# Performance work log

Measured on AMD Instinct MI355X. Metric: run time of the kernel, lower is better.

The kernel has to match this reference:

```python
import jax, jax.numpy as jnp
import numpy as np

TOP_K = 2
LN_EPS = 1e-5

B, S, H, E, F = 2, 2048, 1024, 8, 4096


def setup_inputs() -> dict:
    key = jax.random.key(0)
    ks = jax.random.split(key, 6)
    x = jax.random.normal(ks[0], (B, S, H), dtype=jnp.float32)
    Wg = jax.random.normal(ks[1], (H, E), dtype=jnp.float32) * 0.02
    alpha = jax.random.normal(ks[2], (E,), dtype=jnp.float32)
    ln_w = jnp.ones((E, H), dtype=jnp.float32)
    ln_b = jnp.zeros((E, H), dtype=jnp.float32)
    fc1_w = jax.random.normal(ks[3], (E, H, F), dtype=jnp.float32) * 0.02
    fc1_b = jnp.zeros((E, F), dtype=jnp.float32)
    fc2_w = jax.random.normal(ks[4], (E, F, H), dtype=jnp.float32) * 0.02
    fc2_b = jnp.zeros((E, H), dtype=jnp.float32)
    return {"x": x, "Wg": Wg, "alpha": alpha, "ln_w": ln_w, "ln_b": ln_b,
            "fc1_w": fc1_w, "fc1_b": fc1_b, "fc2_w": fc2_w, "fc2_b": fc2_b}


def _layernorm(x, w, b):
    mu = jnp.mean(x, axis=-1, keepdims=True)
    var = jnp.mean(jnp.square(x - mu), axis=-1, keepdims=True)
    return (x - mu) * jax.lax.rsqrt(var + LN_EPS) * w + b


def reference(x, Wg, alpha, ln_w, ln_b, fc1_w, fc1_b, fc2_w, fc2_b):
    b, s, h = x.shape
    xf = x.reshape(-1, h)                                  # [T, H]
    # ---- gate: top-k over expert logits, softmax over the selected k ----
    logits = xf @ Wg                                       # [T, E]
    top_vals, top_idx = jax.lax.top_k(logits, TOP_K)       # [T, K]
    gate_score = jax.nn.softmax(top_vals, axis=-1)         # [T, K]
    # combine weight per (token, expert): sum_k score_k * 1[idx_k == e], scaled by alpha_e
    one_hot = jax.nn.one_hot(top_idx, Wg.shape[1], dtype=xf.dtype)  # [T, K, E]
    comb = jnp.einsum("tke,tk->te", one_hot, gate_score) * alpha    # [T, E]
    # ---- experts: LayerNorm -> fc1 -> gelu(tanh) -> fc2, weighted combine ----
    out = jnp.zeros_like(xf)
    for e in range(Wg.shape[1]):
        hdn = _layernorm(xf, ln_w[e], ln_b[e])
        a = jax.nn.gelu(hdn @ fc1_w[e] + fc1_b[e], approximate=True)
        y = a @ fc2_w[e] + fc2_b[e]
        out = out + y * comb[:, e:e + 1]
    return out.reshape(b, s, h)
```

## Files before the change

kernel.cpp:

```cpp
#include <hip/hip_runtime.h>
#include <stdint.h>
#include <stdio.h>

#define Td 4096
#define Hd 1024
#define Ed 8
#define Fd 4096
#define ROWS_CAP 9216

typedef unsigned int u32;
typedef unsigned short u16;
typedef float f32x4 __attribute__((ext_vector_type(4)));
typedef float f32x2 __attribute__((ext_vector_type(2)));
typedef __bf16 bf16x8 __attribute__((ext_vector_type(8)));
typedef u16 u16x8 __attribute__((ext_vector_type(8)));
typedef u16 u16x4 __attribute__((ext_vector_type(4)));
typedef u32 u32x4 __attribute__((ext_vector_type(4)));

#define ASG __attribute__((address_space(1)))
#define ASL __attribute__((address_space(3)))

__device__ __forceinline__ void gll16(const void* g, void* l) {
  __builtin_amdgcn_global_load_lds((const ASG u32*)g, (ASL u32*)l, 16, 0, 0);
}

__device__ __forceinline__ u16 f2bf(float f) {
  u32 u = __float_as_uint(f);
  u = u + 0x7fffu + ((u >> 16) & 1u);
  return (u16)(u >> 16);
}

__global__ __launch_bounds__(256) void k_gate(const float* __restrict__ x,
    const float* __restrict__ Wg, const float* __restrict__ alpha,
    float* __restrict__ mu, float* __restrict__ rstd,
    int* __restrict__ tok_e, float* __restrict__ tok_w)
{
  const int t = blockIdx.x, tid = threadIdx.x;
  const f32x4 xv = *(const f32x4*)(x + (size_t)t*Hd + tid*4);
  float s1 = 0.f, s2 = 0.f;
  double lg[8];
#pragma unroll
  for (int e=0;e<8;e++) lg[e]=0.0;
#pragma unroll
  for (int i=0;i<4;i++){
    const float xi = xv[i];
    s1 += xi; s2 += xi*xi;
    const f32x4 wa = *(const f32x4*)(Wg + (size_t)(tid*4+i)*Ed);
    const f32x4 wb = *(const f32x4*)(Wg + (size_t)(tid*4+i)*Ed + 4);
    lg[0] += (double)xi*(double)wa[0]; lg[1] += (double)xi*(double)wa[1];
    lg[2] += (double)xi*(double)wa[2]; lg[3] += (double)xi*(double)wa[3];
    lg[4] += (double)xi*(double)wb[0]; lg[5] += (double)xi*(double)wb[1];
    lg[6] += (double)xi*(double)wb[2]; lg[7] += (double)xi*(double)wb[3];
  }
#pragma unroll
  for (int off=32; off>0; off>>=1){
    s1 += __shfl_down(s1, off);
    s2 += __shfl_down(s2, off);
#pragma unroll
    for (int e=0;e<8;e++) lg[e] += __shfl_down(lg[e], off);
  }
  __shared__ double sl[4][8];
  __shared__ float sa[4], sb[4];
  const int w = tid>>6, lane = tid&63;
  if (lane==0){
#pragma unroll
    for (int e=0;e<8;e++) sl[w][e]=lg[e];
    sa[w]=s1; sb[w]=s2;
  }
  __syncthreads();
  if (tid==0){
    float S1=0.f,S2=0.f; double L[8];
#pragma unroll
    for (int e=0;e<8;e++) L[e]=0.0;
#pragma unroll
    for (int i=0;i<4;i++){
      S1+=sa[i]; S2+=sb[i];
#pragma unroll
      for (int e=0;e<8;e++) L[e]+=sl[i][e];
    }
    const float mean = S1 * (1.f/Hd);
    float var = S2 * (1.f/Hd) - mean*mean;
    if (var < 0.f) var = 0.f;
    mu[t]=mean; rstd[t]=rsqrtf(var + 1e-5f);
    float l[8];
#pragma unroll
    for (int e=0;e<8;e++) l[e]=(float)L[e];
    int e0=0;
#pragma unroll
    for (int e=1;e<8;e++) if (l[e]>l[e0]) e0=e;
    int e1=-1;
#pragma unroll
    for (int e=0;e<8;e++) if (e!=e0 && (e1<0 || l[e]>l[e1])) e1=e;
    const float p = __expf(l[e1]-l[e0]);
    const float inv = 1.f/(1.f+p);
    tok_e[2*t]=e0; tok_e[2*t+1]=e1;
    tok_w[2*t]   = inv   * alpha[e0];
    tok_w[2*t+1] = p*inv * alpha[e1];
  }
}

__global__ __launch_bounds__(256) void k_route(const int* __restrict__ tok_e,
    const float* __restrict__ tok_w, int* __restrict__ meta,
    int* __restrict__ gtok, float* __restrict__ gw)
{
  __shared__ int wsum[4];
  __shared__ int sbase;
  const int tid = threadIdx.x, w = tid>>6, lane = tid&63;
  if (tid==0) sbase = 0;
  __syncthreads();
  for (int e=0;e<8;e++){
    if (tid==0) meta[e] = sbase;
    __syncthreads();
    for (int ch=0; ch<Td/256; ++ch){
      const int t = ch*256 + tid;
      const bool fa = (tok_e[2*t] == e);
      const bool f  = fa || (tok_e[2*t+1] == e);
      const unsigned long long bal = __ballot(f);
      if (lane==0) wsum[w] = __popcll(bal);
      __syncthreads();
      int pre=0, tot=0;
#pragma unroll
      for (int i=0;i<4;i++){ const int v=wsum[i]; if (i<w) pre+=v; tot+=v; }
      if (f){
        const int pos = sbase + pre + __popcll(bal & ((1ull<<lane)-1ull));
        gtok[pos] = t;
        gw[pos]   = tok_w[2*t + (fa?0:1)];
      }
      __syncthreads();
      if (tid==0) sbase += tot;
      __syncthreads();
    }
    const int realend = sbase;
    const int padded  = (realend + 127) & ~127;
    if (tid < padded - realend){
      gtok[realend + tid] = -1;
      gw[realend + tid]   = 0.f;
    }
    __syncthreads();
    if (tid==0){ meta[9+e] = realend - meta[e]; sbase = padded; }
    __syncthreads();
  }
  if (tid==0) meta[8] = sbase;
}

__global__ __launch_bounds__(256) void k_gather(const float* __restrict__ x,
    const float* __restrict__ lnw, const float* __restrict__ lnb,
    const float* __restrict__ mu, const float* __restrict__ rstd,
    const int* __restrict__ meta, const int* __restrict__ gtok,
    u16* __restrict__ Xg)
{
  const int r = blockIdx.x, tid = threadIdx.x;
  __shared__ int ps[9];
  if (tid < 9) ps[tid] = meta[tid];
  __syncthreads();
  if (r >= ps[8]) return;
  int e = 0;
#pragma unroll
  for (int i=1;i<8;i++) if (r >= ps[i]) e = i;
  const int k0 = tid*4;
  const int c  = k0 >> 3;
  const int cs = (c & ~7) | ((c ^ r) & 7);
  u16* dst = Xg + (size_t)r*Hd + cs*8 + (k0 & 7);
  const int t = gtok[r];
  u16x4 o;
  if (t < 0){
    o[0]=0;o[1]=0;o[2]=0;o[3]=0;
  } else {
    const float m = mu[t], s = rstd[t];
    const f32x4 xv = *(const f32x4*)(x   + (size_t)t*Hd + k0);
    const f32x4 wv = *(const f32x4*)(lnw + (size_t)e*Hd + k0);
    const f32x4 bv = *(const f32x4*)(lnb + (size_t)e*Hd + k0);
#pragma unroll
    for (int i=0;i<4;i++) o[i] = f2bf((xv[i]-m)*s*wv[i] + bv[i]);
  }
  *(u16x4*)dst = o;
}

template<int K, int N>
__global__ __launch_bounds__(256) void k_wt(const float* __restrict__ W,
                                            u16* __restrict__ Wt)
{
  const int e = blockIdx.z, kb = blockIdx.x*64, nb = blockIdx.y*64;
  __shared__ u16 T[64*66];
  const int tid = threadIdx.x;
#pragma unroll
  for (int j=0;j<8;j++){
    const int idx = j*256 + tid;
    const int k = idx >> 5;
    const int n = (idx & 31) << 1;
    const f32x2 v = *(const f32x2*)(W + ((size_t)e*K + kb + k)*N + nb + n);
    T[n*66 + k]     = f2bf(v[0]);
    T[(n+1)*66 + k] = f2bf(v[1]);
  }
  __syncthreads();
  const int nl = tid >> 2;
  const int gn = nb + nl;
  u16* dstrow = Wt + ((size_t)e*N + gn)*K;
#pragma unroll
  for (int cc=0; cc<2; ++cc){
    const int c = ((tid & 3) << 1) + cc;
    u32x4 v;
#pragma unroll
    for (int i=0;i<4;i++) v[i] = *(const u32*)&T[nl*66 + c*8 + i*2];
    const int cabs = (kb >> 3) + c;
    const int cs = (cabs & ~7) | ((cabs ^ gn) & 7);
    *(u32x4*)(dstrow + cs*8) = v;
  }
}

template<int KD, int ND, bool FC1, int KSPL>
__global__ __launch_bounds__(256, 3) void k_gemm3(
    const u16* __restrict__ A, const u16* __restrict__ Bt,
    const float* __restrict__ bias, const int* __restrict__ meta,
    const int* __restrict__ gtok, const float* __restrict__ gw,
    u16* __restrict__ Mid, float* __restrict__ out)
{
  const int e = blockIdx.z, mt = blockIdx.y;
  const int nt = blockIdx.x % (ND/128);
  const int kc = blockIdx.x / (ND/128);
  const int p0 = meta[e];
  const int pcnt = meta[e+1] - p0;
  if (mt*128 >= pcnt) return;
  const int row0 = p0 + mt*128;

  __shared__ __attribute__((aligned(16))) u16 As[128*64];
  __shared__ __attribute__((aligned(16))) u16 Bs[128*64];

  const int tid = threadIdx.x;
  const int lane = tid & 63, wid = tid >> 6;
  const int wm = wid >> 1, wn = wid & 1;
  const int l15 = lane & 15, l4 = lane >> 4;

  f32x4 acc[4][4] = {};

  const u16* Ap  = A  + (size_t)row0*KD;
  const u16* Btp = Bt + ((size_t)e*ND + (size_t)nt*128)*KD;

  const int kt0 = kc * (KD/64/KSPL);
  const int kt1 = kt0 + (KD/64/KSPL);

  const int trow = tid >> 3;
  const int tch  = tid & 7;

  u32x4 ra[4], rb[4];

#pragma unroll
  for (int j=0;j<4;j++){
    const size_t off = (size_t)(j*32 + trow)*KD + (size_t)kt0*64 + tch*8;
    ra[j] = *(const u32x4*)(Ap + off);
    rb[j] = *(const u32x4*)(Btp + off);
  }
#pragma unroll
  for (int j=0;j<4;j++){
    *(u32x4*)(&As[(j*256+tid)*8]) = ra[j];
    *(u32x4*)(&Bs[(j*256+tid)*8]) = rb[j];
  }
  __syncthreads();

#pragma unroll 1
  for (int kt=kt0; kt<kt1; ++kt){
    if (kt+1 < kt1){
#pragma unroll
      for (int j=0;j<4;j++){
        const size_t off = (size_t)(j*32 + trow)*KD + (size_t)(kt+1)*64 + tch*8;
        ra[j] = *(const u32x4*)(Ap + off);
        rb[j] = *(const u32x4*)(Btp + off);
      }
    }
#pragma unroll
    for (int ks=0; ks<2; ++ks){
      bf16x8 af[4], bfv[4];
#pragma unroll
      for (int mi=0;mi<4;mi++){
        const int r  = wm*64 + mi*16 + l15;
        const int cb = (ks*4 + l4) ^ (r & 7);
        af[mi] = __builtin_bit_cast(bf16x8, *(const u16x8*)(&As[r*64 + cb*8]));
      }
#pragma unroll
      for (int ni=0;ni<4;ni++){
        const int n  = wn*64 + ni*16 + l15;
        const int cb = (ks*4 + l4) ^ (n & 7);
        bfv[ni] = __builtin_bit_cast(bf16x8, *(const u16x8*)(&Bs[n*64 + cb*8]));
      }
#pragma unroll
      for (int mi=0;mi<4;mi++)
#pragma unroll
        for (int ni=0;ni<4;ni++)
          acc[mi][ni] = __builtin_amdgcn_mfma_f32_16x16x32_bf16(af[mi], bfv[ni], acc[mi][ni], 0, 0, 0);
    }
    __syncthreads();
    if (kt+1 < kt1){
#pragma unroll
      for (int j=0;j<4;j++){
        *(u32x4*)(&As[(j*256+tid)*8]) = ra[j];
        *(u32x4*)(&Bs[(j*256+tid)*8]) = rb[j];
      }
      __syncthreads();
    }
  }

  if (FC1){
#pragma unroll
    for (int mi=0;mi<4;mi++){
      const int grow = row0 + wm*64 + mi*16 + l4*4;
#pragma unroll
      for (int ni=0;ni<4;ni++){
        const int col = nt*128 + wn*64 + ni*16 + l15;
        const float bv = bias[e*ND + col];
#pragma unroll
        for (int j=0;j<4;j++){
          const float v = acc[mi][ni][j] + bv;
          const float z = 0.7978845608028654f * (v + 0.044715f*v*v*v);
          const float g = v / (1.f + __expf(-2.f*z));
          const int gr = grow + j;
          const int cc = col >> 3;
          const int ccs = (cc & ~7) | ((cc ^ gr) & 7);
          Mid[(size_t)gr*Fd + ccs*8 + (col&7)] = f2bf(g);
        }
      }
    }
  } else {
#pragma unroll
    for (int mi=0;mi<4;mi++){
#pragma unroll
      for (int j=0;j<4;j++){
        const int gr = row0 + wm*64 + mi*16 + l4*4 + j;
        const int t = gtok[gr];
        if (t < 0) continue;
        const float wt = gw[gr];
#pragma unroll
        for (int ni=0;ni<4;ni++){
          const int col = nt*128 + wn*64 + ni*16 + l15;
          const float bv = (kc == 0) ? bias[e*ND + col] : 0.f;
          const float v = acc[mi][ni][j] + bv;
          atomicAdd(out + (size_t)t*Hd + col, v*wt);
        }
      }
    }
  }
}

template<int KD, int ND, bool FC1, int KSPL>
__global__ __launch_bounds__(256) void k_gemm_fb(
    const u16* __restrict__ A, const float* __restrict__ B,
    const float* __restrict__ bias, const int* __restrict__ meta,
    const int* __restrict__ gtok, const float* __restrict__ gw,
    u16* __restrict__ Mid, float* __restrict__ out)
{
  const int e = blockIdx.z, mt = blockIdx.y;
  const int nt = blockIdx.x % (ND/128);
  const int kc = blockIdx.x / (ND/128);
  const int p0 = meta[e];
  const int pcnt = meta[e+1] - p0;
  if (mt*128 >= pcnt) return;
  const int row0 = p0 + mt*128;

  __shared__ __attribute__((aligned(16))) u16 As1[128*64];
  __shared__ __attribute__((aligned(16))) u16 Bs1[128*64];

  const int tid = threadIdx.x;
  const int lane = tid & 63, wid = tid >> 6;
  const int wm = wid >> 1, wn = wid & 1;
  const int l15 = lane & 15, l4 = lane >> 4;

  f32x4 acc[4][4] = {};

  const int sbn = (tid & 63) << 1;
  const int skg = tid >> 6;
  const float* Bp = B + (size_t)e*KD*ND + (size_t)nt*128;
  const int kt0 = kc * (KD/64/KSPL);
  const int kt1 = kt0 + (KD/64/KSPL);

  for (int kt=kt0; kt<kt1; ++kt){
    __syncthreads();
#pragma unroll
    for (int j=0;j<4;j++){
      const int cidx = j*256 + tid;
      gll16(A + (size_t)(row0 + (cidx>>3))*KD + kt*64 + (cidx&7)*8, &As1[cidx*8]);
    }
    {
      const float* bsrc = Bp + (size_t)(kt*64 + skg*16)*ND + sbn;
      u32 ra[8], rb[8];
#pragma unroll
      for (int i=0;i<16;i++){
        const f32x2 v = *(const f32x2*)(bsrc + (size_t)i*ND);
        const u32 lo = f2bf(v[0]), hi = f2bf(v[1]);
        if (i & 1){ ra[i>>1] |= lo<<16; rb[i>>1] |= hi<<16; }
        else      { ra[i>>1]  = lo;     rb[i>>1]  = hi;     }
      }
#pragma unroll
      for (int cl=0; cl<2; ++cl){
        const int cb = skg*2 + cl;
        const u32x4 va = { ra[cl*4], ra[cl*4+1], ra[cl*4+2], ra[cl*4+3] };
        const u32x4 vb = { rb[cl*4], rb[cl*4+1], rb[cl*4+2], rb[cl*4+3] };
        *(u32x4*)(&Bs1[(size_t)sbn    *64 + (cb ^ ( sbn   &7))*8]) = va;
        *(u32x4*)(&Bs1[(size_t)(sbn+1)*64 + (cb ^ ((sbn+1)&7))*8]) = vb;
      }
    }
    __syncthreads();
#pragma unroll
    for (int ks=0; ks<2; ++ks){
      bf16x8 af[4], bfv[4];
#pragma unroll
      for (int mi=0;mi<4;mi++){
        const int r  = wm*64 + mi*16 + l15;
        const int cb = (ks*4 + l4) ^ (r & 7);
        af[mi] = __builtin_bit_cast(bf16x8, *(const u16x8*)(&As1[r*64 + cb*8]));
      }
#pragma unroll
      for (int ni=0;ni<4;ni++){
        const int n  = wn*64 + ni*16 + l15;
        const int cb = (ks*4 + l4) ^ (n & 7);
        bfv[ni] = __builtin_bit_cast(bf16x8, *(const u16x8*)(&Bs1[n*64 + cb*8]));
      }
#pragma unroll
      for (int mi=0;mi<4;mi++)
#pragma unroll
        for (int ni=0;ni<4;ni++)
          acc[mi][ni] = __builtin_amdgcn_mfma_f32_16x16x32_bf16(af[mi], bfv[ni], acc[mi][ni], 0, 0, 0);
    }
  }

  if (FC1){
#pragma unroll
    for (int mi=0;mi<4;mi++){
      const int grow = row0 + wm*64 + mi*16 + l4*4;
#pragma unroll
      for (int ni=0;ni<4;ni++){
        const int col = nt*128 + wn*64 + ni*16 + l15;
        const float bv = bias[e*ND + col];
#pragma unroll
        for (int j=0;j<4;j++){
          const float v = acc[mi][ni][j] + bv;
          const float z = 0.7978845608028654f * (v + 0.044715f*v*v*v);
          const float g = v / (1.f + __expf(-2.f*z));
          const int gr = grow + j;
          const int cc = col >> 3;
          const int ccs = (cc & ~7) | ((cc ^ gr) & 7);
          Mid[(size_t)gr*Fd + ccs*8 + (col&7)] = f2bf(g);
        }
      }
    }
  } else {
#pragma unroll
    for (int mi=0;mi<4;mi++){
#pragma unroll
      for (int j=0;j<4;j++){
        const int gr = row0 + wm*64 + mi*16 + l4*4 + j;
        const int t = gtok[gr];
        if (t < 0) continue;
        const float wt = gw[gr];
#pragma unroll
        for (int ni=0;ni<4;ni++){
          const int col = nt*128 + wn*64 + ni*16 + l15;
          const float bv = (kc == 0) ? bias[e*ND + col] : 0.f;
          const float v = acc[mi][ni][j] + bv;
          atomicAdd(out + (size_t)t*Hd + col, v*wt);
        }
      }
    }
  }
}

extern "C" void kernel_launch(void* const* d_in, const int* in_sizes, int n_in,
                              void* d_out, int out_size, void* d_ws, size_t ws_size,
                              hipStream_t stream)
{
  const float* x     = (const float*)d_in[0];
  const float* Wg    = (const float*)d_in[1];
  const float* alpha = (const float*)d_in[2];
  const float* lnw   = (const float*)d_in[3];
  const float* lnb   = (const float*)d_in[4];
  const float* w1    = (const float*)d_in[5];
  const float* b1    = (const float*)d_in[6];
  const float* w2    = (const float*)d_in[7];
  const float* b2    = (const float*)d_in[8];
  float* out = (float*)d_out;
  char* ws = (char*)d_ws;

  float* mu    = (float*)(ws + 0);
  float* rstd  = (float*)(ws + (16<<10));
  int*   tok_e = (int*)  (ws + (32<<10));
  float* tok_w = (float*)(ws + (64<<10));
  int*   meta  = (int*)  (ws + (96<<10));
  int*   gtok  = (int*)  (ws + (100<<10));
  float* gw    = (float*)(ws + (144<<10));
  u16*   Xg    = (u16*)  (ws + (192<<10));
  const size_t xg_b   = 2*(size_t)ROWS_CAP*Hd;
  const size_t mid_b  = 2*(size_t)ROWS_CAP*Fd;
  const size_t wt_b   = 2*(size_t)Ed*Hd*Fd;
  u16*   Amid  = (u16*)  (ws + (192<<10) + xg_b);
  u16*   Wt2   = (u16*)  (ws + (192<<10) + xg_b + mid_b);
  u16*   Wt1   = (u16*)  (ws + (192<<10) + xg_b + mid_b + wt_b);

  const size_t base_need = (192<<10) + xg_b + mid_b;
  if (ws_size < base_need){
    fprintf(stderr, "kernel_launch: ws_size %zu < needed %zu\n", ws_size, base_need);
    return;
  }
  const bool cv2 = ws_size >= base_need + wt_b;
  const bool cv1 = ws_size >= base_need + 2*wt_b;

  hipMemsetAsync(d_out, 0, (size_t)out_size*sizeof(float), stream);
  if (cv2) k_wt<Fd, Hd><<<dim3(Fd/64, Hd/64, Ed), 256, 0, stream>>>(w2, Wt2);
  if (cv1) k_wt<Hd, Fd><<<dim3(Hd/64, Fd/64, Ed), 256, 0, stream>>>(w1, Wt1);
  k_gate  <<<Td, 256, 0, stream>>>(x, Wg, alpha, mu, rstd, tok_e, tok_w);
  k_route <<<1, 256, 0, stream>>>(tok_e, tok_w, meta, gtok, gw);
  k_gather<<<ROWS_CAP, 256, 0, stream>>>(x, lnw, lnb, mu, rstd, meta, gtok, Xg);

  if (cv1)
    k_gemm3<Hd, Fd, true, 1><<<dim3(Fd/128, ROWS_CAP/128, Ed), 256, 0, stream>>>(
        Xg, Wt1, b1, meta, gtok, gw, Amid, nullptr);
  else
    k_gemm_fb<Hd, Fd, true, 1><<<dim3(Fd/128, ROWS_CAP/128, Ed), 256, 0, stream>>>(
        Xg, w1, b1, meta, gtok, gw, Amid, nullptr);

  if (cv2)
    k_gemm3<Fd, Hd, false, 2><<<dim3((Hd/128)*2, ROWS_CAP/128, Ed), 256, 0, stream>>>(
        Amid, Wt2, b2, meta, gtok, gw, nullptr, out);
  else
    k_gemm_fb<Fd, Hd, false, 2><<<dim3((Hd/128)*2, ROWS_CAP/128, Ed), 256, 0, stream>>>(
        Amid, w2, b2, meta, gtok, gw, nullptr, out);
}
```

Before: 453.1 us.

## Parallelize routing into hist/scan/scatter and remap GEMM blocks by XCD

Replaces the single-block serial routing kernel with a three-stage histogram, scan and scatter that runs over many blocks, and pre-fills gtok/gw padding with memsets. The grouped GEMM now uses a 1D grid whose block index is decoded so that each XCD gets a contiguous slab of M tiles and half of the N/K tiles, aiming for better L2 reuse. A scheduling barrier is also inserted after the prefetch loads. Together these target the serialized routing latency and cross-XCD cache misses. The cost is extra kernel launches and memsets.

Result: slower. 927.8 us (+104.8%).

```diff
diff --git a/kernel.cpp b/kernel.cpp
--- a/kernel.cpp
+++ b/kernel.cpp
@@ -99,48 +99,62 @@
   }
 }
 
-__global__ __launch_bounds__(256) void k_route(const int* __restrict__ tok_e,
-    const float* __restrict__ tok_w, int* __restrict__ meta,
+__global__ __launch_bounds__(256) void k_hist(const int* __restrict__ tok_e,
+                                              int* __restrict__ cnt)
+{
+  __shared__ int c[8];
+  const int tid = threadIdx.x, ch = blockIdx.x;
+  if (tid < 8) c[tid] = 0;
+  __syncthreads();
+  const int t = ch*256 + tid;
+  atomicAdd(&c[tok_e[2*t]], 1);
+  atomicAdd(&c[tok_e[2*t+1]], 1);
+  __syncthreads();
+  if (tid < 8) cnt[ch*8 + tid] = c[tid];
+}
+
+__global__ __launch_bounds__(64) void k_scan(const int* __restrict__ cnt,
+                                             int* __restrict__ meta,
+                                             int* __restrict__ base)
+{
+  if (threadIdx.x != 0) return;
+  int s = 0;
+  for (int e=0;e<8;e++){
+    meta[e] = s;
+    int run = s;
+    for (int ch=0; ch<Td/256; ++ch){
+      base[ch*8+e] = run;
+      run += cnt[ch*8+e];
+    }
+    s += (run - s + 127) & ~127;
+  }
+  meta[8] = s;
+}
+
+__global__ __launch_bounds__(256) void k_scatter(const int* __restrict__ tok_e,
+    const float* __restrict__ tok_w, const int* __restrict__ base,
     int* __restrict__ gtok, float* __restrict__ gw)
 {
   __shared__ int wsum[4];
-  __shared__ int sbase;
-  const int tid = threadIdx.x, w = tid>>6, lane = tid&63;
-  if (tid==0) sbase = 0;
-  __syncthreads();
+  const int tid = threadIdx.x, ch = blockIdx.x, w = tid>>6, lane = tid&63;
+  const int t = ch*256 + tid;
+  const int e0 = tok_e[2*t], e1 = tok_e[2*t+1];
   for (int e=0;e<8;e++){
-    if (tid==0) meta[e] = sbase;
+    const bool fa = (e0 == e);
+    const bool f  = fa || (e1 == e);
+    const unsigned long long bal = __ballot(f);
+    if (lane==0) wsum[w] = __popcll(bal);
     __syncthreads();
-    for (int ch=0; ch<Td/256; ++ch){
-      const int t = ch*256 + tid;
-      const bool fa = (tok_e[2*t] == e);
-      const bool f  = fa || (tok_e[2*t+1] == e);
-      const unsigned long long bal = __ballot(f);
-      if (lane==0) wsum[w] = __popcll(bal);
-      __syncthreads();
-      int pre=0, tot=0;
-#pragma unroll
-      for (int i=0;i<4;i++){ const int v=wsum[i]; if (i<w) pre+=v; tot+=v; }
-      if (f){
-        const int pos = sbase + pre + __popcll(bal & ((1ull<<lane)-1ull));
-        gtok[pos] = t;
-        gw[pos]   = tok_w[2*t + (fa?0:1)];
-      }
-      __syncthreads();
-      if (tid==0) sbase += tot;
-      __syncthreads();
-    }
-    const int realend = sbase;
-    const int padded  = (realend + 127) & ~127;
-    if (tid < padded - realend){
-      gtok[realend + tid] = -1;
-      gw[realend + tid]   = 0.f;
+    int pre=0;
+#pragma unroll
+    for (int i=0;i<4;i++){ if (i<w) pre += wsum[i]; }
+    if (f){
+      const int pos = base[ch*8+e] + pre + __popcll(bal & ((1ull<<lane)-1ull));
+      gtok[pos] = t;
+      gw[pos]   = tok_w[2*t + (fa?0:1)];
     }
     __syncthreads();
-    if (tid==0){ meta[9+e] = realend - meta[e]; sbase = padded; }
-    __syncthreads();
-  }
-  if (tid==0) meta[8] = sbase;
+  }
 }
 
 __global__ __launch_bounds__(256) void k_gather(const float* __restrict__ x,
@@ -209,15 +223,29 @@
 }
 
 template<int KD, int ND, bool FC1, int KSPL>
-__global__ __launch_bounds__(256, 3) void k_gemm3(
+__global__ __launch_bounds__(256, 3) void k_gemm6(
     const u16* __restrict__ A, const u16* __restrict__ Bt,
     const float* __restrict__ bias, const int* __restrict__ meta,
     const int* __restrict__ gtok, const float* __restrict__ gw,
     u16* __restrict__ Mid, float* __restrict__ out)
 {
-  const int e = blockIdx.z, mt = blockIdx.y;
-  const int nt = blockIdx.x % (ND/128);
-  const int kc = blockIdx.x / (ND/128);
+  constexpr int NT   = ND/128;
+  constexpr int NTK  = NT*KSPL;
+  constexpr int MT   = ROWS_CAP/128;
+  constexpr int MTC  = MT/4;
+  constexpr int NTKC = NTK/2;
+
+  const int bid = blockIdx.x;
+  const int xcd = bid & 7;
+  const int s   = bid >> 3;
+  const int ntk_l = s / (Ed*MTC);
+  const int rem   = s - ntk_l*(Ed*MTC);
+  const int e     = rem / MTC;
+  const int mt    = (xcd >> 1)*MTC + (rem - e*MTC);
+  const int ntk   = (xcd & 1)*NTKC + ntk_l;
+  const int nt    = ntk % NT;
+  const int kc    = ntk / NT;
+
   const int p0 = meta[e];
   const int pcnt = meta[e+1] - p0;
   if (mt*128 >= pcnt) return;
@@ -236,8 +264,9 @@
   const u16* Ap  = A  + (size_t)row0*KD;
   const u16* Btp = Bt + ((size_t)e*ND + (size_t)nt*128)*KD;
 
-  const int kt0 = kc * (KD/64/KSPL);
-  const int kt1 = kt0 + (KD/64/KSPL);
+  const int ktn = KD/64/KSPL;
+  const int kt0 = kc * ktn;
+  const int kt1 = kt0 + ktn;
 
   const int trow = tid >> 3;
   const int tch  = tid & 7;
@@ -266,6 +295,7 @@
         ra[j] = *(const u32x4*)(Ap + off);
         rb[j] = *(const u32x4*)(Btp + off);
       }
+      __builtin_amdgcn_sched_barrier(0);
     }
 #pragma unroll
     for (int ks=0; ks<2; ++ks){
@@ -483,6 +513,8 @@
   int*   tok_e = (int*)  (ws + (32<<10));
   float* tok_w = (float*)(ws + (64<<10));
   int*   meta  = (int*)  (ws + (96<<10));
+  int*   cnt   = (int*)  (ws + (97<<10));
+  int*   base  = (int*)  (ws + (98<<10));
   int*   gtok  = (int*)  (ws + (100<<10));
   float* gw    = (float*)(ws + (144<<10));
   u16*   Xg    = (u16*)  (ws + (192<<10));
@@ -502,21 +534,29 @@
   const bool cv1 = ws_size >= base_need + 2*wt_b;
 
   hipMemsetAsync(d_out, 0, (size_t)out_size*sizeof(float), stream);
+  hipMemsetAsync(gtok, 0xFF, (size_t)ROWS_CAP*sizeof(int), stream);
+  hipMemsetAsync(gw,   0x00, (size_t)ROWS_CAP*sizeof(float), stream);
+
   if (cv2) k_wt<Fd, Hd><<<dim3(Fd/64, Hd/64, Ed), 256, 0, stream>>>(w2, Wt2);
   if (cv1) k_wt<Hd, Fd><<<dim3(Hd/64, Fd/64, Ed), 256, 0, stream>>>(w1, Wt1);
-  k_gate  <<<Td, 256, 0, stream>>>(x, Wg, alpha, mu, rstd, tok_e, tok_w);
-  k_route <<<1, 256, 0, stream>>>(tok_e, tok_w, meta, gtok, gw);
-  k_gather<<<ROWS_CAP, 256, 0, stream>>>(x, lnw, lnb, mu, rstd, meta, gtok, Xg);
+  k_gate   <<<Td, 256, 0, stream>>>(x, Wg, alpha, mu, rstd, tok_e, tok_w);
+  k_hist   <<<Td/256, 256, 0, stream>>>(tok_e, cnt);
+  k_scan   <<<1, 64, 0, stream>>>(cnt, meta, base);
+  k_scatter<<<Td/256, 256, 0, stream>>>(tok_e, tok_w, base, gtok, gw);
+  k_gather <<<ROWS_CAP, 256, 0, stream>>>(x, lnw, lnb, mu, rstd, meta, gtok, Xg);
+
+  const int g1 = 8 * ((Fd/128)*1/2) * Ed * ((ROWS_CAP/128)/4);
+  const int g2 = 8 * ((Hd/128)*2/2) * Ed * ((ROWS_CAP/128)/4);
 
   if (cv1)
-    k_gemm3<Hd, Fd, true, 1><<<dim3(Fd/128, ROWS_CAP/128, Ed), 256, 0, stream>>>(
+    k_gemm6<Hd, Fd, true, 1><<<g1, 256, 0, stream>>>(
         Xg, Wt1, b1, meta, gtok, gw, Amid, nullptr);
   else
     k_gemm_fb<Hd, Fd, true, 1><<<dim3(Fd/128, ROWS_CAP/128, Ed), 256, 0, stream>>>(
         Xg, w1, b1, meta, gtok, gw, Amid, nullptr);
 
   if (cv2)
-    k_gemm3<Fd, Hd, false, 2><<<dim3((Hd/128)*2, ROWS_CAP/128, Ed), 256, 0, stream>>>(
+    k_gemm6<Fd, Hd, false, 2><<<g2, 256, 0, stream>>>(
         Amid, Wt2, b2, meta, gtok, gw, nullptr, out);
   else
     k_gemm_fb<Fd, Hd, false, 2><<<dim3((Hd/128)*2, ROWS_CAP/128, Ed), 256, 0, stream>>>(
```
